# Performance work log

Hardware: AMD Instinct MI355X
Metric: run time of the kernel (lower is better)

The kernel has to match this reference:

```python
import jax, jax.numpy as jnp
import numpy as np

B, L, V, A = 4096, 64, 50000, 1000
E, H, G, F2 = 32, 32, 256, 512


def _xavier(k, shape):
    fan_out, fan_in = shape
    a = np.sqrt(6.0 / (fan_in + fan_out)).astype(np.float32)
    return jax.random.uniform(k, shape, jnp.float32, -a, a)


def setup_inputs() -> dict:
    key = jax.random.key(0)
    ks = jax.random.split(key, 32)
    inp = {}
    inp["q"] = jax.random.randint(ks[0], (B, L), 0, V)
    for i in range(8):
        inp[f"sf{i}"] = jax.random.randint(ks[1 + i], (B, L), 0, V)
    inp["emb"] = _xavier(ks[9], (V, E))
    # torch LSTM weight layout: [4H, in] with gate order i,f,g,o; biases init to 0
    inp["q_Wih"] = _xavier(ks[10], (4 * H, E))
    inp["q_Whh"] = _xavier(ks[11], (4 * H, H))
    inp["q_b"] = jnp.zeros((4 * H,), jnp.float32)
    inp["sf_Wih"] = _xavier(ks[12], (4 * H, E))
    inp["sf_Whh"] = _xavier(ks[13], (4 * H, H))
    inp["sf_b"] = jnp.zeros((4 * H,), jnp.float32)
    inp["g1_W"] = _xavier(ks[14], (G, 2 * H + 1)); inp["g1_b"] = jnp.zeros((G,), jnp.float32)
    inp["g2_W"] = _xavier(ks[15], (G, G)); inp["g2_b"] = jnp.zeros((G,), jnp.float32)
    inp["g3_W"] = _xavier(ks[16], (G, G)); inp["g3_b"] = jnp.zeros((G,), jnp.float32)
    inp["g4_W"] = _xavier(ks[17], (G, G)); inp["g4_b"] = jnp.zeros((G,), jnp.float32)
    inp["f1_W"] = _xavier(ks[18], (G, G)); inp["f1_b"] = jnp.zeros((G,), jnp.float32)
    inp["f2_W"] = _xavier(ks[19], (F2, G)); inp["f2_b"] = jnp.zeros((F2,), jnp.float32)
    inp["f3_W"] = _xavier(ks[20], (A, F2)); inp["f3_b"] = jnp.zeros((A,), jnp.float32)
    return inp


def _lstm_last(x, Wih, Whh, b):
    """x: [L, N, E] -> final hidden state [N, H]. Torch gate order i,f,g,o."""
    n = x.shape[1]
    h_dim = Whh.shape[1]
    def step(carry, xt):
        h, c = carry
        gates = xt @ Wih.T + h @ Whh.T + b  # [N, 4H]
        i, f, g, o = jnp.split(gates, 4, axis=-1)
        c = jax.nn.sigmoid(f) * c + jax.nn.sigmoid(i) * jnp.tanh(g)
        h = jax.nn.sigmoid(o) * jnp.tanh(c)
        return (h, c), None
    init = (jnp.zeros((n, h_dim), x.dtype), jnp.zeros((n, h_dim), x.dtype))
    (h, _), _ = jax.lax.scan(step, init, x)
    return h


def _lin(x, W, b):
    return x @ W.T + b


def reference(q, sf0, sf1, sf2, sf3, sf4, sf5, sf6, sf7,
              emb, q_Wih, q_Whh, q_b, sf_Wih, sf_Whh, sf_b,
              g1_W, g1_b, g2_W, g2_b, g3_W, g3_b, g4_W, g4_b,
              f1_W, f1_b, f2_W, f2_b, f3_W, f3_b):
    # dropout in eval mode (identity)
    b, l = q.shape
    qe = emb[q].transpose(1, 0, 2)  # [L, B, E]
    hq = _lstm_last(qe, q_Wih, q_Whh, q_b)  # [B, H]

    sf = jnp.stack([sf0, sf1, sf2, sf3, sf4, sf5, sf6, sf7])  # [8, B, L]
    sfe = emb[sf]  # [8, B, L, E]
    sfe = sfe.transpose(2, 0, 1, 3).reshape(l, 8 * b, emb.shape[1])  # one fused LSTM over 8*B
    hs = _lstm_last(sfe, sf_Wih, sf_Whh, sf_b).reshape(8, b, -1)  # [8, B, H]

    pos = jnp.broadcast_to(jnp.arange(8, dtype=hs.dtype)[:, None, None], (8, b, 1))
    x = jnp.concatenate([hs, jnp.broadcast_to(hq, (8, b, hq.shape[-1])), pos], axis=-1)  # [8, B, 65]
    x = jax.nn.relu(_lin(x, g1_W, g1_b))
    x = jax.nn.relu(_lin(x, g2_W, g2_b))
    x = jax.nn.relu(_lin(x, g3_W, g3_b))
    x = jax.nn.relu(_lin(x, g4_W, g4_b))
    g_o = x.sum(axis=0)  # [B, 256] segment-sum over the 8 relations

    x = jax.nn.relu(_lin(g_o, f1_W, f1_b))
    x = jax.nn.relu(_lin(x, f2_W, f2_b))
    return _lin(x, f3_W, f3_b)  # [B, A]
```

## Files before the change

### kernel.cpp

```cpp
#include <hip/hip_runtime.h>
#include <stdint.h>
#include <stddef.h>

typedef __fp16 f16;
typedef __attribute__((ext_vector_type(8))) __fp16 half8;
typedef __attribute__((ext_vector_type(4))) __fp16 half4;
typedef __attribute__((ext_vector_type(4))) float f32x4;
typedef unsigned int u32;
typedef __attribute__((ext_vector_type(2))) u32 u32x2;
typedef __attribute__((ext_vector_type(4))) u32 u32x4;

static __device__ __forceinline__ f32x4 mfma16(half8 a, half8 b, f32x4 c) {
    return __builtin_amdgcn_mfma_f32_16x16x32_f16(a, b, c, 0, 0, 0);
}
static __device__ __forceinline__ float fexp2(float x) { float r; asm("v_exp_f32 %0, %1" : "=v"(r) : "v"(x)); return r; }
static __device__ __forceinline__ float frcp(float x)  { float r; asm("v_rcp_f32 %0, %1" : "=v"(r) : "v"(x)); return r; }

static constexpr float L2E  = 1.4426950408889634f;
static constexpr float L2E2 = 2.8853900817779268f;

static constexpr int LDA = 264;
static constexpr int LDF2 = 520;

static constexpr size_t OFF_EMB   = 0;
static constexpr size_t OFF_WQIH  = 3200000;
static constexpr size_t OFF_WQHH  = OFF_WQIH + 8192;
static constexpr size_t OFF_WSIH  = OFF_WQHH + 8192;
static constexpr size_t OFF_WSHH  = OFF_WSIH + 8192;
static constexpr size_t OFF_BQ    = OFF_WSHH + 8192;
static constexpr size_t OFF_BS    = OFF_BQ + 512;
static constexpr size_t OFF_G1WP  = OFF_BS + 512;
static constexpr size_t OFF_BIAS8 = OFF_G1WP + 32768;
static constexpr size_t OFF_G2W   = OFF_BIAS8 + 8192;
static constexpr size_t OFF_G3W   = OFF_G2W + 131072;
static constexpr size_t OFF_G4W   = OFF_G3W + 131072;
static constexpr size_t OFF_F1W   = OFF_G4W + 131072;
static constexpr size_t OFF_F2W   = OFF_F1W + 131072;
static constexpr size_t OFF_F3W   = OFF_F2W + 262144;
static constexpr size_t OFF_HS    = OFF_F3W + 1024000;
static constexpr size_t OFF_HQ    = OFF_HS + 2097152;
static constexpr size_t OFF_ACT2  = OFF_HQ + 262144;
static constexpr size_t WS_NEED   = OFF_ACT2 + 16777216;

struct CvtJobs { const float* src[7]; f16* dst[7]; int n[7]; };

__global__ __launch_bounds__(256) void cvt_prep(
    CvtJobs j,
    const float* __restrict__ g1W, const float* __restrict__ g1b,
    f16* __restrict__ wp, float* __restrict__ bias8,
    const float* __restrict__ qWih, const float* __restrict__ qWhh, const float* __restrict__ qb,
    const float* __restrict__ sWih, const float* __restrict__ sWhh, const float* __restrict__ sb,
    f16* __restrict__ wqih, f16* __restrict__ wqhh, float* __restrict__ bq,
    f16* __restrict__ wsih, f16* __restrict__ wshh, float* __restrict__ bs)
{
    int t = threadIdx.x;
    if (blockIdx.y < 7) {
        int jb = blockIdx.y;
        int i = (blockIdx.x * 256 + t) * 8;
        if (i >= j.n[jb]) return;
        const float* s = j.src[jb] + i;
        f32x4 a = *(const f32x4*)s;
        f32x4 b = *(const f32x4*)(s + 4);
        half8 o;
        o[0]=(f16)a[0]; o[1]=(f16)a[1]; o[2]=(f16)a[2]; o[3]=(f16)a[3];
        o[4]=(f16)b[0]; o[5]=(f16)b[1]; o[6]=(f16)b[2]; o[7]=(f16)b[3];
        *(half8*)(j.dst[jb] + i) = o;
        return;
    }
    if (blockIdx.x == 0) {
        int col = t;
        for (int k = 0; k < 64; k++) wp[col * 64 + k] = (f16)g1W[col * 65 + k];
        float wpos = g1W[col * 65 + 64];
        float b = g1b[col];
        for (int i = 0; i < 8; i++) bias8[i * 256 + col] = b + (float)i * wpos;
    } else if (blockIdx.x == 1) {
        for (int i = t; i < 4096; i += 256) {
            int row = i >> 5;
            float s = (row < 64 || row >= 96) ? -L2E : L2E2;
            wqih[i] = (f16)(qWih[i] * s);
            wqhh[i] = (f16)(qWhh[i] * s);
            wsih[i] = (f16)(sWih[i] * s);
            wshh[i] = (f16)(sWhh[i] * s);
        }
        if (t < 128) {
            float s = (t < 64 || t >= 96) ? -L2E : L2E2;
            bq[t] = qb[t] * s;
            bs[t] = sb[t] * s;
        }
    }
}

struct SfPtrs { const int* p[8]; };

__global__ __launch_bounds__(64) void lstm_kernel(
    SfPtrs sf, const int* __restrict__ qtok, const f16* __restrict__ emb_h,
    const f16* __restrict__ wih_sf, const f16* __restrict__ whh_sf, const float* __restrict__ b_sf,
    const f16* __restrict__ wih_q,  const f16* __restrict__ whh_q,  const float* __restrict__ b_q,
    f16* __restrict__ hs_out, f16* __restrict__ hq_out)
{
    int lane = threadIdx.x;
    int c15 = lane & 15, kq = lane >> 4;
    int sbase = blockIdx.x * 16;
    bool isq = sbase >= 32768;
    const f16* wih = isq ? wih_q : wih_sf;
    const f16* whh = isq ? whh_q : whh_sf;
    const float* bvec = isq ? b_q : b_sf;

    half8 wi[8], wh[8];
    f32x4 bc[8];
    #pragma unroll
    for (int n = 0; n < 8; n++) {
        wi[n] = *(const half8*)(wih + (n * 16 + c15) * 32 + kq * 8);
        wh[n] = *(const half8*)(whh + (n * 16 + c15) * 32 + kq * 8);
        bc[n] = *(const f32x4*)(bvec + n * 16 + kq * 4);
    }
    int sg = sbase + c15;
    const int* tp;
    if (isq) tp = qtok + (sg - 32768) * 64;
    else     tp = sf.p[sg >> 12] + (sg & 4095) * 64;

    int i1 = (c15 + ((kq & 1) << 5)) << 2;
    int i2 = i1 + 64;
    bool hi = kq >= 2;

    float cst[2][4] = {};
    half8 hf = {};
    half8 xf = *(const half8*)(emb_h + (size_t)tp[0] * 32 + kq * 8);

    #pragma unroll 1
    for (int t = 0; t < 64; t++) {
        f32x4 acc[8];
        #pragma unroll
        for (int n = 0; n < 8; n++) acc[n] = mfma16(wi[n], xf, bc[n]);
        #pragma unroll
        for (int n = 0; n < 8; n++) acc[n] = mfma16(wh[n], hf, acc[n]);
        if (t < 63) {
            int tk = tp[t + 1];
            xf = *(const half8*)(emb_h + (size_t)tk * 32 + kq * 8);
        }
        half4 hp0, hp1;
        #pragma unroll
        for (int jh = 0; jh < 2; jh++) {
            #pragma unroll
            for (int r = 0; r < 4; r++) {
                float ei = fexp2(acc[0 + jh][r]);
                float ef = fexp2(acc[2 + jh][r]);
                float eg = fexp2(acc[4 + jh][r]);
                float eo = fexp2(acc[6 + jh][r]);
                float t1 = 1.f + ei, t2 = 1.f + ef, t5 = 1.f + eo;
                float eg1 = eg + 1.f, egm = eg - 1.f;
                float t1e = t1 * eg1;
                float num = fmaf(egm, t2, cst[jh][r] * t1e);
                float cn  = num * frcp(t1e * t2);
                cst[jh][r] = cn;
                float ec  = fexp2(cn * L2E2);
                float hv  = (ec - 1.f) * frcp((ec + 1.f) * t5);
                if (jh == 0) hp0[r] = (f16)hv; else hp1[r] = (f16)hv;
            }
        }
        u32x2 pa = __builtin_bit_cast(u32x2, hp0);
        u32x2 pb = __builtin_bit_cast(u32x2, hp1);
        int ra0 = __builtin_amdgcn_ds_bpermute(i1, (int)pa.x);
        int ra1 = __builtin_amdgcn_ds_bpermute(i1, (int)pa.y);
        int rb0 = __builtin_amdgcn_ds_bpermute(i1, (int)pb.x);
        int rb1 = __builtin_amdgcn_ds_bpermute(i1, (int)pb.y);
        int ra2 = __builtin_amdgcn_ds_bpermute(i2, (int)pa.x);
        int ra3 = __builtin_amdgcn_ds_bpermute(i2, (int)pa.y);
        int rb2 = __builtin_amdgcn_ds_bpermute(i2, (int)pb.x);
        int rb3 = __builtin_amdgcn_ds_bpermute(i2, (int)pb.y);
        u32x4 w;
        w.x = (u32)(hi ? rb0 : ra0);
        w.y = (u32)(hi ? rb1 : ra1);
        w.z = (u32)(hi ? rb2 : ra2);
        w.w = (u32)(hi ? rb3 : ra3);
        hf = __builtin_bit_cast(half8, w);
    }
    if (isq) *(half8*)(hq_out + (size_t)(sg - 32768) * 32 + kq * 8) = hf;
    else     *(half8*)(hs_out + (size_t)sg * 32 + kq * 8) = hf;
}

template<bool TOGLOBAL>
static __device__ __forceinline__ void layer256(
    const f16 (* __restrict__ src)[LDA], f16 (* __restrict__ dst)[LDA],
    const f16* __restrict__ W, const float* __restrict__ bias,
    f16* __restrict__ gout, int m0, int wm, int wn, int c15, int kq)
{
    f32x4 acc[2][4];
    #pragma unroll
    for (int a = 0; a < 2; a++)
        #pragma unroll
        for (int b = 0; b < 4; b++) acc[a][b] = (f32x4){0.f, 0.f, 0.f, 0.f};
    #pragma unroll
    for (int k0 = 0; k0 < 8; k0++) {
        half8 av[2], bv[4];
        #pragma unroll
        for (int fm = 0; fm < 2; fm++) av[fm] = *(const half8*)(&src[wm * 32 + fm * 16 + c15][k0 * 32 + kq * 8]);
        #pragma unroll
        for (int fn = 0; fn < 4; fn++) bv[fn] = *(const half8*)(W + (size_t)(wn * 64 + fn * 16 + c15) * 256 + k0 * 32 + kq * 8);
        #pragma unroll
        for (int fm = 0; fm < 2; fm++)
            #pragma unroll
            for (int fn = 0; fn < 4; fn++) acc[fm][fn] = mfma16(av[fm], bv[fn], acc[fm][fn]);
    }
    #pragma unroll
    for (int fn = 0; fn < 4; fn++) {
        int col = wn * 64 + fn * 16 + c15;
        float bb = bias[col];
        #pragma unroll
        for (int fm = 0; fm < 2; fm++)
            #pragma unroll
            for (int r = 0; r < 4; r++) {
                float v = fmaxf(acc[fm][fn][r] + bb, 0.f);
                int row = wm * 32 + fm * 16 + kq * 4 + r;
                if (TOGLOBAL) gout[(size_t)(m0 + row) * 256 + col] = (f16)v;
                else          dst[row][col] = (f16)v;
            }
    }
}

__global__ __launch_bounds__(512) void gemm_g1234(
    const f16* __restrict__ hs, const f16* __restrict__ hq,
    const f16* __restrict__ g1wp, const float* __restrict__ bias8,
    const f16* __restrict__ g2w, const float* __restrict__ g2b,
    const f16* __restrict__ g3w, const float* __restrict__ g3b,
    const f16* __restrict__ g4w, const float* __restrict__ g4b,
    f16* __restrict__ act2)
{
    __shared__ __align__(16) f16 actA[64][LDA];
    __shared__ __align__(16) f16 actB[64][LDA];
    const int wv = threadIdx.x >> 6, lane = threadIdx.x & 63;
    const int c15 = lane & 15, kq = lane >> 4;
    const int wm = wv >> 2, wn = wv & 3;
    const int m0 = blockIdx.x * 64;
    const float* brow = bias8 + ((m0 >> 12) << 8);

    {
        f32x4 acc[2][4];
        #pragma unroll
        for (int a = 0; a < 2; a++)
            #pragma unroll
            for (int b = 0; b < 4; b++) acc[a][b] = (f32x4){0.f, 0.f, 0.f, 0.f};
        half8 av[2], bv[4];
        #pragma unroll
        for (int fm = 0; fm < 2; fm++) av[fm] = *(const half8*)(hs + (size_t)(m0 + wm * 32 + fm * 16 + c15) * 32 + kq * 8);
        #pragma unroll
        for (int fn = 0; fn < 4; fn++) bv[fn] = *(const half8*)(g1wp + (size_t)(wn * 64 + fn * 16 + c15) * 64 + kq * 8);
        #pragma unroll
        for (int fm = 0; fm < 2; fm++)
            #pragma unroll
            for (int fn = 0; fn < 4; fn++) acc[fm][fn] = mfma16(av[fm], bv[fn], acc[fm][fn]);
        #pragma unroll
        for (int fm = 0; fm < 2; fm++) av[fm] = *(const half8*)(hq + (size_t)((m0 + wm * 32 + fm * 16 + c15) & 4095) * 32 + kq * 8);
        #pragma unroll
        for (int fn = 0; fn < 4; fn++) bv[fn] = *(const half8*)(g1wp + (size_t)(wn * 64 + fn * 16 + c15) * 64 + 32 + kq * 8);
        #pragma unroll
        for (int fm = 0; fm < 2; fm++)
            #pragma unroll
            for (int fn = 0; fn < 4; fn++) acc[fm][fn] = mfma16(av[fm], bv[fn], acc[fm][fn]);
        #pragma unroll
        for (int fn = 0; fn < 4; fn++) {
            int col = wn * 64 + fn * 16 + c15;
            float bb = brow[col];
            #pragma unroll
            for (int fm = 0; fm < 2; fm++)
                #pragma unroll
                for (int r = 0; r < 4; r++)
                    actA[wm * 32 + fm * 16 + kq * 4 + r][col] = (f16)fmaxf(acc[fm][fn][r] + bb, 0.f);
        }
    }
    __syncthreads();
    layer256<false>(actA, actB, g2w, g2b, nullptr, m0, wm, wn, c15, kq);
    __syncthreads();
    layer256<false>(actB, actA, g3w, g3b, nullptr, m0, wm, wn, c15, kq);
    __syncthreads();
    layer256<true>(actA, actB, g4w, g4b, act2, m0, wm, wn, c15, kq);
}

__global__ __launch_bounds__(512) void f123s_kernel(
    const f16* __restrict__ act2,
    const f16* __restrict__ f1w, const float* __restrict__ f1b,
    const f16* __restrict__ f2w, const float* __restrict__ f2b,
    const f16* __restrict__ f3w, const float* __restrict__ f3b,
    float* __restrict__ out)
{
    __shared__ __align__(16) f16 smbuf[16][LDA];
    __shared__ __align__(16) f16 f1buf[16][LDA];
    __shared__ __align__(16) f16 f2buf[16][LDF2];
    const int b0 = blockIdx.x * 16;

    {
        int r = threadIdx.x >> 5, cb = (threadIdx.x & 31) * 8;
        float s[8] = {};
        #pragma unroll
        for (int i = 0; i < 8; i++) {
            half8 v = *(const half8*)(act2 + ((size_t)(i * 4096 + b0 + r)) * 256 + cb);
            #pragma unroll
            for (int q = 0; q < 8; q++) s[q] += (float)v[q];
        }
        half8 o;
        #pragma unroll
        for (int q = 0; q < 8; q++) o[q] = (f16)s[q];
        *(half8*)(&smbuf[r][cb]) = o;
    }
    __syncthreads();
    const int wv = threadIdx.x >> 6, lane = threadIdx.x & 63;
    const int c15 = lane & 15, kq = lane >> 4;

    {
        f32x4 acc[2];
        acc[0] = (f32x4){0.f, 0.f, 0.f, 0.f}; acc[1] = acc[0];
        #pragma unroll
        for (int k0 = 0; k0 < 8; k0++) {
            half8 a = *(const half8*)(&smbuf[c15][k0 * 32 + kq * 8]);
            #pragma unroll
            for (int fn = 0; fn < 2; fn++) {
                half8 bv = *(const half8*)(f1w + (size_t)(wv * 32 + fn * 16 + c15) * 256 + k0 * 32 + kq * 8);
                acc[fn] = mfma16(a, bv, acc[fn]);
            }
        }
        #pragma unroll
        for (int fn = 0; fn < 2; fn++) {
            int col = wv * 32 + fn * 16 + c15;
            float bb = f1b[col];
            #pragma unroll
            for (int r = 0; r < 4; r++)
                f1buf[kq * 4 + r][col] = (f16)fmaxf(acc[fn][r] + bb, 0.f);
        }
    }
    __syncthreads();
    {
        f32x4 acc[4];
        #pragma unroll
        for (int b = 0; b < 4; b++) acc[b] = (f32x4){0.f, 0.f, 0.f, 0.f};
        #pragma unroll
        for (int k0 = 0; k0 < 8; k0++) {
            half8 a = *(const half8*)(&f1buf[c15][k0 * 32 + kq * 8]);
            #pragma unroll
            for (int fn = 0; fn < 4; fn++) {
                half8 bv = *(const half8*)(f2w + (size_t)(wv * 64 + fn * 16 + c15) * 256 + k0 * 32 + kq * 8);
                acc[fn] = mfma16(a, bv, acc[fn]);
            }
        }
        #pragma unroll
        for (int fn = 0; fn < 4; fn++) {
            int col = wv * 64 + fn * 16 + c15;
            float bb = f2b[col];
            #pragma unroll
            for (int r = 0; r < 4; r++)
                f2buf[kq * 4 + r][col] = (f16)fmaxf(acc[fn][r] + bb, 0.f);
        }
    }
    __syncthreads();
    {
        f32x4 acc[8];
        #pragma unroll
        for (int b = 0; b < 8; b++) acc[b] = (f32x4){0.f, 0.f, 0.f, 0.f};
        #pragma unroll
        for (int k0 = 0; k0 < 16; k0++) {
            half8 a = *(const half8*)(&f2buf[c15][k0 * 32 + kq * 8]);
            #pragma unroll
            for (int fn = 0; fn < 8; fn++) {
                int col = wv * 128 + fn * 16 + c15;
                int cl = col < 1000 ? col : 999;
                half8 bv = *(const half8*)(f3w + (size_t)cl * 512 + k0 * 32 + kq * 8);
                acc[fn] = mfma16(a, bv, acc[fn]);
            }
        }
        #pragma unroll
        for (int fn = 0; fn < 8; fn++) {
            int col = wv * 128 + fn * 16 + c15;
            if (col < 1000) {
                float bb = f3b[col];
                #pragma unroll
                for (int r = 0; r < 4; r++)
                    out[(size_t)(b0 + kq * 4 + r) * 1000 + col] = acc[fn][r] + bb;
            }
        }
    }
}

extern "C" void kernel_launch(void* const* d_in, const int* in_sizes, int n_in,
                              void* d_out, int out_size, void* d_ws, size_t ws_size,
                              hipStream_t stream)
{
    if (ws_size < WS_NEED) return;
    const int* q_tok = (const int*)d_in[0];
    SfPtrs sf;
    for (int i = 0; i < 8; i++) sf.p[i] = (const int*)d_in[1 + i];
    const float* emb_f = (const float*)d_in[9];
    const float* qWih = (const float*)d_in[10];
    const float* qWhh = (const float*)d_in[11];
    const float* q_b  = (const float*)d_in[12];
    const float* sWih = (const float*)d_in[13];
    const float* sWhh = (const float*)d_in[14];
    const float* s_b  = (const float*)d_in[15];
    const float* g1W  = (const float*)d_in[16];
    const float* g1b  = (const float*)d_in[17];
    const float* g2W  = (const float*)d_in[18];
    const float* g2b  = (const float*)d_in[19];
    const float* g3W  = (const float*)d_in[20];
    const float* g3b  = (const float*)d_in[21];
    const float* g4W  = (const float*)d_in[22];
    const float* g4b  = (const float*)d_in[23];
    const float* f1W  = (const float*)d_in[24];
    const float* f1b  = (const float*)d_in[25];
    const float* f2W  = (const float*)d_in[26];
    const float* f2b  = (const float*)d_in[27];
    const float* f3W  = (const float*)d_in[28];
    const float* f3b  = (const float*)d_in[29];

    char* ws = (char*)d_ws;
    f16* emb_h = (f16*)(ws + OFF_EMB);
    f16* wqih  = (f16*)(ws + OFF_WQIH);
    f16* wqhh  = (f16*)(ws + OFF_WQHH);
    f16* wsih  = (f16*)(ws + OFF_WSIH);
    f16* wshh  = (f16*)(ws + OFF_WSHH);
    float* bq  = (float*)(ws + OFF_BQ);
    float* bs  = (float*)(ws + OFF_BS);
    f16* g1wp  = (f16*)(ws + OFF_G1WP);
    float* bias8 = (float*)(ws + OFF_BIAS8);
    f16* g2w = (f16*)(ws + OFF_G2W);
    f16* g3w = (f16*)(ws + OFF_G3W);
    f16* g4w = (f16*)(ws + OFF_G4W);
    f16* f1w = (f16*)(ws + OFF_F1W);
    f16* f2w = (f16*)(ws + OFF_F2W);
    f16* f3w = (f16*)(ws + OFF_F3W);
    f16* hs  = (f16*)(ws + OFF_HS);
    f16* hq  = (f16*)(ws + OFF_HQ);
    f16* act2 = (f16*)(ws + OFF_ACT2);

    CvtJobs cj;
    const float* srcs[7] = {emb_f, g2W, g3W, g4W, f1W, f2W, f3W};
    f16* dsts[7]         = {emb_h, g2w, g3w, g4w, f1w, f2w, f3w};
    int ns[7] = {1600000, 65536, 65536, 65536, 65536, 131072, 512000};
    for (int i = 0; i < 7; i++) { cj.src[i] = srcs[i]; cj.dst[i] = dsts[i]; cj.n[i] = ns[i]; }

    cvt_prep<<<dim3(782, 8), 256, 0, stream>>>(cj, g1W, g1b, g1wp, bias8,
                                               qWih, qWhh, q_b, sWih, sWhh, s_b,
                                               wqih, wqhh, bq, wsih, wshh, bs);
    lstm_kernel<<<2304, 64, 0, stream>>>(sf, q_tok, emb_h, wsih, wshh, bs, wqih, wqhh, bq, hs, hq);
    gemm_g1234<<<512, 512, 0, stream>>>(hs, hq, g1wp, bias8, g2w, g2b, g3w, g3b, g4w, g4b, act2);
    f123s_kernel<<<256, 512, 0, stream>>>(act2, f1w, f1b, f2w, f2b, f3w, f3b, (float*)d_out);
}
```

Baseline: 344.2 us.

## Split LSTM gate work across two waves with LDS hidden-state exchange

Each LSTM block now uses two wavefronts, and each wave computes half of the hidden units (4 gate tiles instead of 8). The new hidden state is exchanged through a double-buffered LDS array with a block barrier, replacing the intra-wave bpermute shuffles. This halves the per-wave serial MFMA and transcendental chain on the recurrent critical path and doubles the wave count. In exchange it adds a __syncthreads per timestep plus LDS round-trips, and both waves load the same embedding row redundantly.

Measured after the change: 319.5 us. 1.08x faster.

```diff
diff --git a/kernel.cpp b/kernel.cpp
--- a/kernel.cpp
+++ b/kernel.cpp
@@ -7,8 +7,6 @@
 typedef __attribute__((ext_vector_type(4))) __fp16 half4;
 typedef __attribute__((ext_vector_type(4))) float f32x4;
 typedef unsigned int u32;
-typedef __attribute__((ext_vector_type(2))) u32 u32x2;
-typedef __attribute__((ext_vector_type(4))) u32 u32x4;
 
 static __device__ __forceinline__ f32x4 mfma16(half8 a, half8 b, f32x4 c) {
     return __builtin_amdgcn_mfma_f32_16x16x32_f16(a, b, c, 0, 0, 0);
@@ -92,13 +90,15 @@
 
 struct SfPtrs { const int* p[8]; };
 
-__global__ __launch_bounds__(64) void lstm_kernel(
+__global__ __launch_bounds__(128) void lstm_kernel(
     SfPtrs sf, const int* __restrict__ qtok, const f16* __restrict__ emb_h,
     const f16* __restrict__ wih_sf, const f16* __restrict__ whh_sf, const float* __restrict__ b_sf,
     const f16* __restrict__ wih_q,  const f16* __restrict__ whh_q,  const float* __restrict__ b_q,
     f16* __restrict__ hs_out, f16* __restrict__ hq_out)
 {
-    int lane = threadIdx.x;
+    __shared__ __align__(16) char hbuf[2][16 * 80];
+    int tid = threadIdx.x;
+    int w = tid >> 6, lane = tid & 63;
     int c15 = lane & 15, kq = lane >> 4;
     int sbase = blockIdx.x * 16;
     bool isq = sbase >= 32768;
@@ -106,77 +106,67 @@
     const f16* whh = isq ? whh_q : whh_sf;
     const float* bvec = isq ? b_q : b_sf;
 
-    half8 wi[8], wh[8];
-    f32x4 bc[8];
+    half8 wi[4], wh[4];
+    f32x4 bc[4];
     #pragma unroll
-    for (int n = 0; n < 8; n++) {
-        wi[n] = *(const half8*)(wih + (n * 16 + c15) * 32 + kq * 8);
-        wh[n] = *(const half8*)(whh + (n * 16 + c15) * 32 + kq * 8);
-        bc[n] = *(const f32x4*)(bvec + n * 16 + kq * 4);
+    for (int jg = 0; jg < 4; jg++) {
+        int row = (2 * jg + w) * 16 + c15;
+        wi[jg] = *(const half8*)(wih + row * 32 + kq * 8);
+        wh[jg] = *(const half8*)(whh + row * 32 + kq * 8);
+        bc[jg] = *(const f32x4*)(bvec + (2 * jg + w) * 16 + kq * 4);
     }
     int sg = sbase + c15;
     const int* tp;
     if (isq) tp = qtok + (sg - 32768) * 64;
     else     tp = sf.p[sg >> 12] + (sg & 4095) * 64;
 
-    int i1 = (c15 + ((kq & 1) << 5)) << 2;
-    int i2 = i1 + 64;
-    bool hi = kq >= 2;
-
-    float cst[2][4] = {};
-    half8 hf = {};
+    for (int i = tid; i < 640; i += 128) ((u32*)hbuf[0])[i] = 0;
+    __syncthreads();
+
+    float cst[4] = {};
+    int rb = 0;
+    const int hoff_r = c15 * 80 + kq * 16;
+    const int hoff_w = c15 * 80 + w * 32 + kq * 8;
+
     half8 xf = *(const half8*)(emb_h + (size_t)tp[0] * 32 + kq * 8);
 
     #pragma unroll 1
     for (int t = 0; t < 64; t++) {
-        f32x4 acc[8];
-        #pragma unroll
-        for (int n = 0; n < 8; n++) acc[n] = mfma16(wi[n], xf, bc[n]);
-        #pragma unroll
-        for (int n = 0; n < 8; n++) acc[n] = mfma16(wh[n], hf, acc[n]);
+        half8 hf = *(const half8*)(hbuf[rb] + hoff_r);
+        f32x4 acc[4];
+        #pragma unroll
+        for (int jg = 0; jg < 4; jg++) acc[jg] = mfma16(wi[jg], xf, bc[jg]);
+        #pragma unroll
+        for (int jg = 0; jg < 4; jg++) acc[jg] = mfma16(wh[jg], hf, acc[jg]);
         if (t < 63) {
             int tk = tp[t + 1];
             xf = *(const half8*)(emb_h + (size_t)tk * 32 + kq * 8);
         }
-        half4 hp0, hp1;
-        #pragma unroll
-        for (int jh = 0; jh < 2; jh++) {
-            #pragma unroll
-            for (int r = 0; r < 4; r++) {
-                float ei = fexp2(acc[0 + jh][r]);
-                float ef = fexp2(acc[2 + jh][r]);
-                float eg = fexp2(acc[4 + jh][r]);
-                float eo = fexp2(acc[6 + jh][r]);
-                float t1 = 1.f + ei, t2 = 1.f + ef, t5 = 1.f + eo;
-                float eg1 = eg + 1.f, egm = eg - 1.f;
-                float t1e = t1 * eg1;
-                float num = fmaf(egm, t2, cst[jh][r] * t1e);
-                float cn  = num * frcp(t1e * t2);
-                cst[jh][r] = cn;
-                float ec  = fexp2(cn * L2E2);
-                float hv  = (ec - 1.f) * frcp((ec + 1.f) * t5);
-                if (jh == 0) hp0[r] = (f16)hv; else hp1[r] = (f16)hv;
-            }
-        }
-        u32x2 pa = __builtin_bit_cast(u32x2, hp0);
-        u32x2 pb = __builtin_bit_cast(u32x2, hp1);
-        int ra0 = __builtin_amdgcn_ds_bpermute(i1, (int)pa.x);
-        int ra1 = __builtin_amdgcn_ds_bpermute(i1, (int)pa.y);
-        int rb0 = __builtin_amdgcn_ds_bpermute(i1, (int)pb.x);
-        int rb1 = __builtin_amdgcn_ds_bpermute(i1, (int)pb.y);
-        int ra2 = __builtin_amdgcn_ds_bpermute(i2, (int)pa.x);
-        int ra3 = __builtin_amdgcn_ds_bpermute(i2, (int)pa.y);
-        int rb2 = __builtin_amdgcn_ds_bpermute(i2, (int)pb.x);
-        int rb3 = __builtin_amdgcn_ds_bpermute(i2, (int)pb.y);
-        u32x4 w;
-        w.x = (u32)(hi ? rb0 : ra0);
-        w.y = (u32)(hi ? rb1 : ra1);
-        w.z = (u32)(hi ? rb2 : ra2);
-        w.w = (u32)(hi ? rb3 : ra3);
-        hf = __builtin_bit_cast(half8, w);
-    }
-    if (isq) *(half8*)(hq_out + (size_t)(sg - 32768) * 32 + kq * 8) = hf;
-    else     *(half8*)(hs_out + (size_t)sg * 32 + kq * 8) = hf;
+        half4 hp;
+        #pragma unroll
+        for (int r = 0; r < 4; r++) {
+            float ei = fexp2(acc[0][r]);
+            float ef = fexp2(acc[1][r]);
+            float eg = fexp2(acc[2][r]);
+            float eo = fexp2(acc[3][r]);
+            float t1 = 1.f + ei, t2 = 1.f + ef, t5 = 1.f + eo;
+            float eg1 = eg + 1.f, egm = eg - 1.f;
+            float t1e = t1 * eg1;
+            float num = fmaf(egm, t2, cst[r] * t1e);
+            float cn  = num * frcp(t1e * t2);
+            cst[r] = cn;
+            float ec  = fexp2(cn * L2E2);
+            hp[r] = (f16)((ec - 1.f) * frcp((ec + 1.f) * t5));
+        }
+        *(half4*)(hbuf[rb ^ 1] + hoff_w) = hp;
+        __syncthreads();
+        rb ^= 1;
+    }
+    if (w == 0) {
+        half8 hv = *(const half8*)(hbuf[rb] + hoff_r);
+        if (isq) *(half8*)(hq_out + (size_t)(sg - 32768) * 32 + kq * 8) = hv;
+        else     *(half8*)(hs_out + (size_t)sg * 32 + kq * 8) = hv;
+    }
 }
 
 template<bool TOGLOBAL>
@@ -438,7 +428,7 @@
     cvt_prep<<<dim3(782, 8), 256, 0, stream>>>(cj, g1W, g1b, g1wp, bias8,
                                                qWih, qWhh, q_b, sWih, sWhh, s_b,
                                                wqih, wqhh, bq, wsih, wshh, bs);
-    lstm_kernel<<<2304, 64, 0, stream>>>(sf, q_tok, emb_h, wsih, wshh, bs, wqih, wqhh, bq, hs, hq);
+    lstm_kernel<<<2304, 128, 0, stream>>>(sf, q_tok, emb_h, wsih, wshh, bs, wqih, wqhh, bq, hs, hq);
     gemm_g1234<<<512, 512, 0, stream>>>(hs, hq, g1wp, bias8, g2w, g2b, g3w, g3b, g4w, g4b, act2);
     f123s_kernel<<<256, 512, 0, stream>>>(act2, f1w, f1b, f2w, f2b, f3w, f3b, (float*)d_out);
 }
```
